# Kernel tuning notes

Measured on AMD Instinct MI355X. Metric: run time of the kernel, lower is better.

## Reference

```python
import jax, jax.numpy as jnp
import numpy as np

INPUT_SIZE = 4
HIDDEN = 2048
OUTPUT_SIZE = 2
NOISE_STD = 0.05
ALPHA = 0.2
RANK = 2
N_SUPPORTS = 2
GDIM = 2 * RANK + INPUT_SIZE  # gaussian_basis_dim default
BATCH = 32
SEQ = 1000


def setup_inputs() -> dict:
    key = jax.random.key(0)
    ks = jax.random.split(key, 8)
    inp = jax.random.normal(ks[0], (BATCH, SEQ, INPUT_SIZE), dtype=jnp.float32)
    noise = jax.random.normal(ks[1], (BATCH, SEQ, HIDDEN), dtype=jnp.float32)
    gaussian_basis = jax.random.normal(ks[2], (GDIM, HIDDEN), dtype=jnp.float32)
    # supports: block indicator masks over hidden units (equal split, weights=None)
    sup = np.zeros((N_SUPPORTS, HIDDEN), dtype=np.float32)
    l = HIDDEN // N_SUPPORTS
    for i in range(N_SUPPORTS):
        sup[i, l * i:l * (i + 1)] = 1.0
    supports = jnp.asarray(sup)
    wi_weights = jax.random.normal(ks[3], (INPUT_SIZE, N_SUPPORTS, GDIM), dtype=jnp.float32)
    m_weights = jax.random.normal(ks[4], (RANK, N_SUPPORTS, GDIM), dtype=jnp.float32) / jnp.sqrt(jnp.float32(HIDDEN))
    n_weights = jax.random.normal(ks[5], (RANK, N_SUPPORTS, GDIM), dtype=jnp.float32) / jnp.sqrt(jnp.float32(HIDDEN))
    wo_weights = jax.random.normal(ks[6], (OUTPUT_SIZE, N_SUPPORTS, GDIM), dtype=jnp.float32) / jnp.float32(HIDDEN)
    wi_biases = jnp.zeros((INPUT_SIZE, N_SUPPORTS), dtype=jnp.float32)
    m_biases = jnp.zeros((RANK, N_SUPPORTS), dtype=jnp.float32)
    n_biases = jnp.zeros((RANK, N_SUPPORTS), dtype=jnp.float32)
    h0_weights = jnp.zeros((N_SUPPORTS, GDIM), dtype=jnp.float32)
    return {
        "input": inp, "noise": noise,
        "wi_weights": wi_weights, "m_weights": m_weights, "n_weights": n_weights,
        "wo_weights": wo_weights, "wi_biases": wi_biases, "m_biases": m_biases,
        "n_biases": n_biases, "h0_weights": h0_weights,
        "gaussian_basis": gaussian_basis, "supports": supports,
    }


def _proxy_params(wi_weights, m_weights, n_weights, wo_weights,
                  wi_biases, m_biases, n_biases, h0_weights,
                  gaussian_basis, supports):
    # (X, S, G) @ (G, H) -> (X, S, H); mask by supports (S, H); sum over S
    def mix(w):
        return jnp.einsum('xsg,gh->xsh', w, gaussian_basis)
    wi = jnp.sum(mix(wi_weights) * supports, axis=1) + wi_biases @ supports      # (I, H)
    m = (jnp.sum(mix(m_weights) * supports, axis=1) + m_biases @ supports).T     # (H, R)
    n = (jnp.sum(mix(n_weights) * supports, axis=1) + n_biases @ supports).T     # (H, R)
    wo = jnp.sum(mix(wo_weights) * supports, axis=1).T                            # (H, O)
    h0 = jnp.sum((h0_weights @ gaussian_basis) * supports, axis=0)                # (H,)
    return wi, m, n, wo, h0


def reference(input, noise, wi_weights, m_weights, n_weights, wo_weights,
              wi_biases, m_biases, n_biases, h0_weights, gaussian_basis, supports):
    wi, m, n, wo, h0 = _proxy_params(wi_weights, m_weights, n_weights, wo_weights,
                                     wi_biases, m_biases, n_biases, h0_weights,
                                     gaussian_basis, supports)
    B = input.shape[0]
    # Precompute external input projection for all steps: (B, T, H)
    xin = jnp.einsum('bti,ih->bth', input, wi)
    h_init = jnp.broadcast_to(h0, (B, h0.shape[0]))
    r_init = jnp.tanh(h_init)

    noise_T = jnp.swapaxes(noise, 0, 1)  # (T, B, H)
    xin_T = jnp.swapaxes(xin, 0, 1)      # (T, B, H)

    def step(carry, xs):
        h, r = carry
        noise_t, xin_t = xs
        h = h + NOISE_STD * noise_t + ALPHA * (-h + (r @ n) @ m.T + xin_t)
        r = jnp.tanh(h)
        return (h, r), r

    _, rs = jax.lax.scan(step, (h_init, r_init), (noise_T, xin_T))  # rs: (T, B, H)
    output = jnp.einsum('tbh,ho->bto', rs, wo)  # (B, T, O)
    return output
```

## Files before the change

kernel.cpp:

```cpp
#include <hip/hip_runtime.h>

#define BATCH 32
#define SEQT 1000
#define INSZ 4
#define HID 2048
#define NOISE_STD 0.05f
#define ALPHA 0.2f
#define ONE_M_ALPHA (1.0f - ALPHA)

#define NTHREADS 512
#define NWAVES 8
#define EPT 4
#define PF 4

typedef float v2f __attribute__((ext_vector_type(2)));

__device__ __forceinline__ v2f vfma(v2f a, v2f b, v2f c) { return a * b + c; }

template<int CTRL>
__device__ __forceinline__ float dpp_add(float x) {
    int s = __builtin_amdgcn_update_dpp(0, __float_as_int(x), CTRL, 0xF, 0xF, true);
    return x + __int_as_float(s);
}

__device__ __forceinline__ float wave_sum64_to_lane63(float x) {
    x = dpp_add<0x111>(x);
    x = dpp_add<0x112>(x);
    x = dpp_add<0x114>(x);
    x = dpp_add<0x118>(x);
    x = dpp_add<0x142>(x);
    x = dpp_add<0x143>(x);
    return x;
}

__device__ __forceinline__ float sum8_to_lane7(float x) {
    x = dpp_add<0x111>(x);
    x = dpp_add<0x112>(x);
    x = dpp_add<0x114>(x);
    return x;
}

__device__ __forceinline__ float read_lane7(float x) {
    return __int_as_float(__builtin_amdgcn_readlane(__float_as_int(x), 7));
}

__device__ __forceinline__ v2f pade_tanh(v2f x) {
    const v2f x2 = x * x;
    const v2f a  = x2 + 105.0f;
    const v2f num = x * vfma(x2, a, v2f{945.0f, 945.0f});
    const v2f c  = vfma(x2, v2f{15.0f, 15.0f}, v2f{420.0f, 420.0f});
    const v2f d  = vfma(x2, c, v2f{945.0f, 945.0f});
    v2f r;
    r.x = num.x * __builtin_amdgcn_rcpf(d.x);
    r.y = num.y * __builtin_amdgcn_rcpf(d.y);
    r.x = fminf(fmaxf(r.x, -1.0f), 1.0f);
    r.y = fminf(fmaxf(r.y, -1.0f), 1.0f);
    return r;
}

__device__ __forceinline__ float pade_tanh_s(float x) {
    const float x2 = x * x;
    const float num = x * fmaf(x2, x2 + 105.0f, 945.0f);
    const float den = fmaf(x2, fmaf(x2, 15.0f, 420.0f), 945.0f);
    float r = num * __builtin_amdgcn_rcpf(den);
    return fminf(fmaxf(r, -1.0f), 1.0f);
}

#define LDS_BARRIER() __asm__ volatile("s_waitcnt lgkmcnt(0)\ns_barrier" ::: "memory")

__global__ __launch_bounds__(NTHREADS)
void rnn_kernel(const float* __restrict__ input,
                const float* __restrict__ noise,
                const float* __restrict__ wi_w,
                const float* __restrict__ m_w,
                const float* __restrict__ n_w,
                const float* __restrict__ wo_w,
                const float* __restrict__ wi_b,
                const float* __restrict__ m_b,
                const float* __restrict__ n_b,
                const float* __restrict__ h0_w,
                const float* __restrict__ gb,
                const float* __restrict__ sup,
                float* __restrict__ out)
{
    __shared__ float4 sIn4[SEQT];
    __shared__ __align__(16) float4 sRed[2][NWAVES];

    const int b    = blockIdx.x;
    const int tid  = threadIdx.x;
    const int wave = tid >> 6;
    const int lane = tid & 63;

    const float4* inRow4 = reinterpret_cast<const float4*>(input + (size_t)b * SEQT * INSZ);
    for (int i = tid; i < SEQT; i += NTHREADS)
        sIn4[i] = inRow4[i];

    v2f wiA[INSZ][2];
    v2f mA0v[2], mA1v[2], n0v[2], n1v[2], wo0v[2], wo1v[2], hv[2];
    v2f q0 = {0.f, 0.f}, q1 = q0, q2 = q0, q3 = q0;

    #pragma unroll
    for (int e = 0; e < EPT; ++e) {
        const int h = tid * 4 + e;
        const int pi = e >> 1, pc = e & 1;
        float gv[8];
        #pragma unroll
        for (int g = 0; g < 8; ++g) gv[g] = gb[g * HID + h];
        const float s0 = sup[h];
        const float s1 = sup[HID + h];

        auto mix = [&](const float* w) -> float {
            float a0 = 0.f, a1 = 0.f;
            #pragma unroll
            for (int g = 0; g < 8; ++g) { a0 += w[g] * gv[g]; a1 += w[8 + g] * gv[g]; }
            return s0 * a0 + s1 * a1;
        };

        #pragma unroll
        for (int i = 0; i < INSZ; ++i)
            wiA[i][pi][pc] = ALPHA * (mix(wi_w + i * 16) + wi_b[i * 2 + 0] * s0 + wi_b[i * 2 + 1] * s1);
        mA0v[pi][pc] = ALPHA * (mix(m_w)      + m_b[0] * s0 + m_b[1] * s1);
        mA1v[pi][pc] = ALPHA * (mix(m_w + 16) + m_b[2] * s0 + m_b[3] * s1);
        const float n0 = mix(n_w)      + n_b[0] * s0 + n_b[1] * s1;
        const float n1 = mix(n_w + 16) + n_b[2] * s0 + n_b[3] * s1;
        const float w0 = mix(wo_w);
        const float w1 = mix(wo_w + 16);
        n0v[pi][pc] = n0;  n1v[pi][pc] = n1;
        wo0v[pi][pc] = w0; wo1v[pi][pc] = w1;
        {
            float a0 = 0.f, a1 = 0.f;
            #pragma unroll
            for (int g = 0; g < 8; ++g) { a0 += h0_w[g] * gv[g]; a1 += h0_w[8 + g] * gv[g]; }
            const float h0v = s0 * a0 + s1 * a1;
            hv[pi][pc] = h0v;
            const float r = pade_tanh_s(h0v);
            q0[pc] += r * n0;  q1[pc] += r * n1;
            q2[pc] += r * w0;  q3[pc] += r * w1;
        }
    }

    const float4* nP4 = reinterpret_cast<const float4*>(noise + (size_t)b * SEQT * HID);
    const int rowStride = HID / 4;
    float4 nb0 = nP4[0 * rowStride + tid];
    float4 nb1 = nP4[1 * rowStride + tid];
    float4 nb2 = nP4[2 * rowStride + tid];
    float4 nb3 = nP4[3 * rowStride + tid];

    float* outRow = out + (size_t)b * SEQT * 2;

    __syncthreads();
    float4 inv0 = sIn4[0];
    float4 inv1 = sIn4[1];
    float4 inv2 = sIn4[2];
    float4 inv3 = sIn4[3];

    float oz = 0.f, ow = 0.f;

    auto do_step = [&](int t, float4& nbuf, float4& invReg) {
        const int par = t & 1;
        const float p0 = q0.x + q0.y, p1 = q1.x + q1.y;
        const float w0 = wave_sum64_to_lane63(p0);
        const float w1 = wave_sum64_to_lane63(p1);
        if (lane == 63) sRed[par][wave] = make_float4(w0, w1, oz, ow);

        LDS_BARRIER();

        const float4 pr = sRed[par][lane & 7];

        const float p2 = q2.x + q2.y, p3 = q3.x + q3.y;
        const float ozn = wave_sum64_to_lane63(p2);
        const float own = wave_sum64_to_lane63(p3);

        const int tpre = (t + PF < SEQT) ? (t + PF) : (SEQT - 1);
        const float4 nv4 = nbuf;
        nbuf = nP4[(size_t)tpre * rowStride + tid];
        const float4 inv = invReg;
        invReg = sIn4[tpre];

        const v2f nlo = {nv4.x, nv4.y}, nhi = {nv4.z, nv4.w};
        v2f acc0 = wiA[0][0] * inv.x;
        v2f acc1 = wiA[0][1] * inv.x;
        acc0 = vfma(wiA[1][0], inv.y, acc0);  acc1 = vfma(wiA[1][1], inv.y, acc1);
        acc0 = vfma(wiA[2][0], inv.z, acc0);  acc1 = vfma(wiA[2][1], inv.z, acc1);
        acc0 = vfma(wiA[3][0], inv.w, acc0);  acc1 = vfma(wiA[3][1], inv.w, acc1);
        acc0 = acc0 + nlo * NOISE_STD;        acc1 = acc1 + nhi * NOISE_STD;
        acc0 = vfma(hv[0], ONE_M_ALPHA, acc0); acc1 = vfma(hv[1], ONE_M_ALPHA, acc1);

        const float y0 = read_lane7(sum8_to_lane7(pr.x));
        const float y1 = read_lane7(sum8_to_lane7(pr.y));

        if (t >= 2 && wave == (t & 7)) {
            const float o0 = sum8_to_lane7(pr.z);
            const float o1 = sum8_to_lane7(pr.w);
            if (lane == 7)
                *reinterpret_cast<float2*>(outRow + (t - 2) * 2) = make_float2(o0, o1);
        }
        oz = ozn; ow = own;

        v2f h2a = vfma(mA1v[0], y1, acc0);
        v2f h2b = vfma(mA1v[1], y1, acc1);
        h2a = vfma(mA0v[0], y0, h2a);
        h2b = vfma(mA0v[1], y0, h2b);
        hv[0] = h2a; hv[1] = h2b;
        const v2f r2a = pade_tanh(h2a);
        const v2f r2b = pade_tanh(h2b);
        q0 = r2a * n0v[0];  q0 = vfma(r2b, n0v[1], q0);
        q1 = r2a * n1v[0];  q1 = vfma(r2b, n1v[1], q1);
        q2 = r2a * wo0v[0]; q2 = vfma(r2b, wo0v[1], q2);
        q3 = r2a * wo1v[0]; q3 = vfma(r2b, wo1v[1], q3);
    };

    for (int t = 0; t < SEQT; t += PF) {
        do_step(t,     nb0, inv0);
        do_step(t + 1, nb1, inv1);
        do_step(t + 2, nb2, inv2);
        do_step(t + 3, nb3, inv3);
    }

    {
        const float p2 = q2.x + q2.y, p3 = q3.x + q3.y;
        const float w2 = wave_sum64_to_lane63(p2);
        const float w3 = wave_sum64_to_lane63(p3);
        if (lane == 63) sRed[0][wave] = make_float4(w2, w3, oz, ow);
        LDS_BARRIER();
        if (wave == 0) {
            const float4 pr = sRed[0][lane & 7];
            const float a999 = sum8_to_lane7(pr.x);
            const float b999 = sum8_to_lane7(pr.y);
            const float a998 = sum8_to_lane7(pr.z);
            const float b998 = sum8_to_lane7(pr.w);
            if (lane == 7) {
                *reinterpret_cast<float2*>(outRow + 998 * 2) = make_float2(a998, b998);
                *reinterpret_cast<float2*>(outRow + 999 * 2) = make_float2(a999, b999);
            }
        }
    }
}

extern "C" void kernel_launch(void* const* d_in, const int* in_sizes, int n_in,
                              void* d_out, int out_size, void* d_ws, size_t ws_size,
                              hipStream_t stream) {
    const float* input = (const float*)d_in[0];
    const float* noise = (const float*)d_in[1];
    const float* wi_w  = (const float*)d_in[2];
    const float* m_w   = (const float*)d_in[3];
    const float* n_w   = (const float*)d_in[4];
    const float* wo_w  = (const float*)d_in[5];
    const float* wi_b  = (const float*)d_in[6];
    const float* m_b   = (const float*)d_in[7];
    const float* n_b   = (const float*)d_in[8];
    const float* h0_w  = (const float*)d_in[9];
    const float* gb    = (const float*)d_in[10];
    const float* sup   = (const float*)d_in[11];
    float* out = (float*)d_out;

    rnn_kernel<<<dim3(BATCH), dim3(NTHREADS), 0, stream>>>(
        input, noise, wi_w, m_w, n_w, wo_w, wi_b, m_b, n_b, h0_w, gb, sup, out);
}
```

Baseline: 871.9 us.

## Hand-code DPP reductions and packed FMA, store full-wave partials to LDS

Replaces the builtin DPP reduction helpers with inline-asm DPP adds that interleave two independent reductions. Every lane now writes its partial to LDS, which removes the lane-63 conditional store, and the cross-wave sum uses a butterfly so every lane holds the result without a readlane. The output partials move to a separate double-buffered LDS array that is read one step later. Inputs are stored pre-duplicated in LDS so that all per-step arithmetic can use explicit v_pk_fma/mul/add. The goal is a shorter serial per-step latency chain; in exchange, inline asm limits compiler scheduling and adds more LDS stores per step.

```diff
diff --git a/kernel.cpp b/kernel.cpp
--- a/kernel.cpp
+++ b/kernel.cpp
@@ -15,44 +15,53 @@
 
 typedef float v2f __attribute__((ext_vector_type(2)));
 
-__device__ __forceinline__ v2f vfma(v2f a, v2f b, v2f c) { return a * b + c; }
-
-template<int CTRL>
-__device__ __forceinline__ float dpp_add(float x) {
-    int s = __builtin_amdgcn_update_dpp(0, __float_as_int(x), CTRL, 0xF, 0xF, true);
-    return x + __int_as_float(s);
-}
-
-__device__ __forceinline__ float wave_sum64_to_lane63(float x) {
-    x = dpp_add<0x111>(x);
-    x = dpp_add<0x112>(x);
-    x = dpp_add<0x114>(x);
-    x = dpp_add<0x118>(x);
-    x = dpp_add<0x142>(x);
-    x = dpp_add<0x143>(x);
-    return x;
-}
-
-__device__ __forceinline__ float sum8_to_lane7(float x) {
-    x = dpp_add<0x111>(x);
-    x = dpp_add<0x112>(x);
-    x = dpp_add<0x114>(x);
-    return x;
-}
-
-__device__ __forceinline__ float read_lane7(float x) {
-    return __int_as_float(__builtin_amdgcn_readlane(__float_as_int(x), 7));
+__device__ __forceinline__ v2f pk_fma(v2f a, v2f b, v2f c) {
+    v2f d; asm("v_pk_fma_f32 %0, %1, %2, %3" : "=v"(d) : "v"(a), "v"(b), "v"(c)); return d;
+}
+__device__ __forceinline__ v2f pk_mul(v2f a, v2f b) {
+    v2f d; asm("v_pk_mul_f32 %0, %1, %2" : "=v"(d) : "v"(a), "v"(b)); return d;
+}
+__device__ __forceinline__ v2f pk_add(v2f a, v2f b) {
+    v2f d; asm("v_pk_add_f32 %0, %1, %2" : "=v"(d) : "v"(a), "v"(b)); return d;
+}
+#define C2(v) (v2f{(v), (v)})
+
+
+__device__ __forceinline__ void tree64_pair(float& a, float& b) {
+    asm("s_nop 1\n\t"
+        "v_add_f32_dpp %0, %0, %0 row_shr:1 row_mask:0xf bank_mask:0xf bound_ctrl:0\n\t"
+        "v_add_f32_dpp %1, %1, %1 row_shr:1 row_mask:0xf bank_mask:0xf bound_ctrl:0\n\t"
+        "v_add_f32_dpp %0, %0, %0 row_shr:2 row_mask:0xf bank_mask:0xf bound_ctrl:0\n\t"
+        "v_add_f32_dpp %1, %1, %1 row_shr:2 row_mask:0xf bank_mask:0xf bound_ctrl:0\n\t"
+        "v_add_f32_dpp %0, %0, %0 row_shr:4 row_mask:0xf bank_mask:0xf bound_ctrl:0\n\t"
+        "v_add_f32_dpp %1, %1, %1 row_shr:4 row_mask:0xf bank_mask:0xf bound_ctrl:0\n\t"
+        "v_add_f32_dpp %0, %0, %0 row_shr:8 row_mask:0xf bank_mask:0xf bound_ctrl:0\n\t"
+        "v_add_f32_dpp %1, %1, %1 row_shr:8 row_mask:0xf bank_mask:0xf bound_ctrl:0\n\t"
+        "v_add_f32_dpp %0, %0, %0 row_bcast:15 row_mask:0xf bank_mask:0xf bound_ctrl:0\n\t"
+        "v_add_f32_dpp %1, %1, %1 row_bcast:15 row_mask:0xf bank_mask:0xf bound_ctrl:0\n\t"
+        "v_add_f32_dpp %0, %0, %0 row_bcast:31 row_mask:0xf bank_mask:0xf bound_ctrl:0\n\t"
+        "v_add_f32_dpp %1, %1, %1 row_bcast:31 row_mask:0xf bank_mask:0xf bound_ctrl:0"
+        : "+v"(a), "+v"(b));
+}
+
+__device__ __forceinline__ void bfly8_pair(float& a, float& b) {
+    asm("s_nop 1\n\t"
+        "v_add_f32_dpp %0, %0, %0 quad_perm:[1,0,3,2] row_mask:0xf bank_mask:0xf\n\t"
+        "v_add_f32_dpp %1, %1, %1 quad_perm:[1,0,3,2] row_mask:0xf bank_mask:0xf\n\t"
+        "v_add_f32_dpp %0, %0, %0 quad_perm:[2,3,0,1] row_mask:0xf bank_mask:0xf\n\t"
+        "v_add_f32_dpp %1, %1, %1 quad_perm:[2,3,0,1] row_mask:0xf bank_mask:0xf\n\t"
+        "v_add_f32_dpp %0, %0, %0 row_half_mirror row_mask:0xf bank_mask:0xf\n\t"
+        "v_add_f32_dpp %1, %1, %1 row_half_mirror row_mask:0xf bank_mask:0xf"
+        : "+v"(a), "+v"(b));
 }
 
 __device__ __forceinline__ v2f pade_tanh(v2f x) {
-    const v2f x2 = x * x;
-    const v2f a  = x2 + 105.0f;
-    const v2f num = x * vfma(x2, a, v2f{945.0f, 945.0f});
-    const v2f c  = vfma(x2, v2f{15.0f, 15.0f}, v2f{420.0f, 420.0f});
-    const v2f d  = vfma(x2, c, v2f{945.0f, 945.0f});
+    const v2f x2  = pk_mul(x, x);
+    const v2f num = pk_mul(x, pk_fma(x2, pk_add(x2, C2(105.0f)), C2(945.0f)));
+    const v2f den = pk_fma(x2, pk_fma(x2, C2(15.0f), C2(420.0f)), C2(945.0f));
     v2f r;
-    r.x = num.x * __builtin_amdgcn_rcpf(d.x);
-    r.y = num.y * __builtin_amdgcn_rcpf(d.y);
+    r.x = num.x * __builtin_amdgcn_rcpf(den.x);
+    r.y = num.y * __builtin_amdgcn_rcpf(den.y);
     r.x = fminf(fmaxf(r.x, -1.0f), 1.0f);
     r.y = fminf(fmaxf(r.y, -1.0f), 1.0f);
     return r;
@@ -83,8 +92,9 @@
                 const float* __restrict__ sup,
                 float* __restrict__ out)
 {
-    __shared__ float4 sIn4[SEQT];
-    __shared__ __align__(16) float4 sRed[2][NWAVES];
+    __shared__ __align__(16) float2 sDup[SEQT][4];
+    __shared__ float2 sW[2][NWAVES][65];
+    __shared__ float2 sO[2][NWAVES][65];
 
     const int b    = blockIdx.x;
     const int tid  = threadIdx.x;
@@ -92,8 +102,13 @@
     const int lane = tid & 63;
 
     const float4* inRow4 = reinterpret_cast<const float4*>(input + (size_t)b * SEQT * INSZ);
-    for (int i = tid; i < SEQT; i += NTHREADS)
-        sIn4[i] = inRow4[i];
+    for (int i = tid; i < SEQT; i += NTHREADS) {
+        const float4 v = inRow4[i];
+        sDup[i][0] = make_float2(v.x, v.x);
+        sDup[i][1] = make_float2(v.y, v.y);
+        sDup[i][2] = make_float2(v.z, v.z);
+        sDup[i][3] = make_float2(v.w, v.w);
+    }
 
     v2f wiA[INSZ][2];
     v2f mA0v[2], mA1v[2], n0v[2], n1v[2], wo0v[2], wo1v[2], hv[2];
@@ -149,90 +164,93 @@
     float* outRow = out + (size_t)b * SEQT * 2;
 
     __syncthreads();
-    float4 inv0 = sIn4[0];
-    float4 inv1 = sIn4[1];
-    float4 inv2 = sIn4[2];
-    float4 inv3 = sIn4[3];
-
-    float oz = 0.f, ow = 0.f;
-
-    auto do_step = [&](int t, float4& nbuf, float4& invReg) {
-        const int par = t & 1;
-        const float p0 = q0.x + q0.y, p1 = q1.x + q1.y;
-        const float w0 = wave_sum64_to_lane63(p0);
-        const float w1 = wave_sum64_to_lane63(p1);
-        if (lane == 63) sRed[par][wave] = make_float4(w0, w1, oz, ow);
+    const float4* dRow = reinterpret_cast<const float4*>(sDup);
+    float4 ivA0 = dRow[0], ivB0 = dRow[1];
+    float4 ivA1 = dRow[2], ivB1 = dRow[3];
+    float4 ivA2 = dRow[4], ivB2 = dRow[5];
+    float4 ivA3 = dRow[6], ivB3 = dRow[7];
+
+    const v2f cNS  = C2(NOISE_STD);
+    const v2f cOMA = C2(ONE_M_ALPHA);
+
+    auto do_step = [&](int t, int PAR, float4& nbuf, float4& ivAreg, float4& ivBreg) {
+        float w0 = q0.x + q0.y;
+        float w1 = q1.x + q1.y;
+        tree64_pair(w0, w1);
+        sW[PAR][wave][lane] = make_float2(w0, w1);
 
         LDS_BARRIER();
 
-        const float4 pr = sRed[par][lane & 7];
-
-        const float p2 = q2.x + q2.y, p3 = q3.x + q3.y;
-        const float ozn = wave_sum64_to_lane63(p2);
-        const float own = wave_sum64_to_lane63(p3);
+        const float2 prw = sW[PAR][lane & 7][63];
+        const float2 pro = sO[PAR ^ 1][lane & 7][63];
+
+        float oz = q2.x + q2.y;
+        float ow = q3.x + q3.y;
+        tree64_pair(oz, ow);
+        sO[PAR][wave][lane] = make_float2(oz, ow);
 
         const int tpre = (t + PF < SEQT) ? (t + PF) : (SEQT - 1);
         const float4 nv4 = nbuf;
         nbuf = nP4[(size_t)tpre * rowStride + tid];
-        const float4 inv = invReg;
-        invReg = sIn4[tpre];
+        const float4 ivA = ivAreg, ivB = ivBreg;
+        ivAreg = dRow[2 * tpre];
+        ivBreg = dRow[2 * tpre + 1];
 
         const v2f nlo = {nv4.x, nv4.y}, nhi = {nv4.z, nv4.w};
-        v2f acc0 = wiA[0][0] * inv.x;
-        v2f acc1 = wiA[0][1] * inv.x;
-        acc0 = vfma(wiA[1][0], inv.y, acc0);  acc1 = vfma(wiA[1][1], inv.y, acc1);
-        acc0 = vfma(wiA[2][0], inv.z, acc0);  acc1 = vfma(wiA[2][1], inv.z, acc1);
-        acc0 = vfma(wiA[3][0], inv.w, acc0);  acc1 = vfma(wiA[3][1], inv.w, acc1);
-        acc0 = acc0 + nlo * NOISE_STD;        acc1 = acc1 + nhi * NOISE_STD;
-        acc0 = vfma(hv[0], ONE_M_ALPHA, acc0); acc1 = vfma(hv[1], ONE_M_ALPHA, acc1);
-
-        const float y0 = read_lane7(sum8_to_lane7(pr.x));
-        const float y1 = read_lane7(sum8_to_lane7(pr.y));
-
-        if (t >= 2 && wave == (t & 7)) {
-            const float o0 = sum8_to_lane7(pr.z);
-            const float o1 = sum8_to_lane7(pr.w);
-            if (lane == 7)
-                *reinterpret_cast<float2*>(outRow + (t - 2) * 2) = make_float2(o0, o1);
-        }
-        oz = ozn; ow = own;
-
-        v2f h2a = vfma(mA1v[0], y1, acc0);
-        v2f h2b = vfma(mA1v[1], y1, acc1);
-        h2a = vfma(mA0v[0], y0, h2a);
-        h2b = vfma(mA0v[1], y0, h2b);
+        const v2f ix = {ivA.x, ivA.y}, iy = {ivA.z, ivA.w};
+        const v2f iz = {ivB.x, ivB.y}, iw = {ivB.z, ivB.w};
+        v2f acc0 = pk_mul(wiA[0][0], ix);
+        v2f acc1 = pk_mul(wiA[0][1], ix);
+        acc0 = pk_fma(wiA[1][0], iy, acc0);  acc1 = pk_fma(wiA[1][1], iy, acc1);
+        acc0 = pk_fma(wiA[2][0], iz, acc0);  acc1 = pk_fma(wiA[2][1], iz, acc1);
+        acc0 = pk_fma(wiA[3][0], iw, acc0);  acc1 = pk_fma(wiA[3][1], iw, acc1);
+        acc0 = pk_fma(nlo, cNS, acc0);       acc1 = pk_fma(nhi, cNS, acc1);
+        acc0 = pk_fma(hv[0], cOMA, acc0);    acc1 = pk_fma(hv[1], cOMA, acc1);
+
+        float y0 = prw.x, y1 = prw.y;
+        bfly8_pair(y0, y1);
+
+        float o0 = pro.x, o1 = pro.y;
+        bfly8_pair(o0, o1);
+        if (t >= 2 && tid == ((t & 7) << 6))
+            *reinterpret_cast<float2*>(outRow + (t - 2) * 2) = make_float2(o0, o1);
+
+        const v2f y0p = {y0, y0}, y1p = {y1, y1};
+        v2f h2a = pk_fma(mA1v[0], y1p, acc0);
+        v2f h2b = pk_fma(mA1v[1], y1p, acc1);
+        h2a = pk_fma(mA0v[0], y0p, h2a);
+        h2b = pk_fma(mA0v[1], y0p, h2b);
         hv[0] = h2a; hv[1] = h2b;
         const v2f r2a = pade_tanh(h2a);
         const v2f r2b = pade_tanh(h2b);
-        q0 = r2a * n0v[0];  q0 = vfma(r2b, n0v[1], q0);
-        q1 = r2a * n1v[0];  q1 = vfma(r2b, n1v[1], q1);
-        q2 = r2a * wo0v[0]; q2 = vfma(r2b, wo0v[1], q2);
-        q3 = r2a * wo1v[0]; q3 = vfma(r2b, wo1v[1], q3);
+        q0 = pk_fma(r2b, n0v[1],  pk_mul(r2a, n0v[0]));
+        q1 = pk_fma(r2b, n1v[1],  pk_mul(r2a, n1v[0]));
+        q2 = pk_fma(r2b, wo0v[1], pk_mul(r2a, wo0v[0]));
+        q3 = pk_fma(r2b, wo1v[1], pk_mul(r2a, wo1v[0]));
     };
 
     for (int t = 0; t < SEQT; t += PF) {
-        do_step(t,     nb0, inv0);
-        do_step(t + 1, nb1, inv1);
-        do_step(t + 2, nb2, inv2);
-        do_step(t + 3, nb3, inv3);
+        do_step(t,     0, nb0, ivA0, ivB0);
+        do_step(t + 1, 1, nb1, ivA1, ivB1);
+        do_step(t + 2, 0, nb2, ivA2, ivB2);
+        do_step(t + 3, 1, nb3, ivA3, ivB3);
     }
 
     {
-        const float p2 = q2.x + q2.y, p3 = q3.x + q3.y;
-        const float w2 = wave_sum64_to_lane63(p2);
-        const float w3 = wave_sum64_to_lane63(p3);
-        if (lane == 63) sRed[0][wave] = make_float4(w2, w3, oz, ow);
+        float a9 = q2.x + q2.y;
+        float b9 = q3.x + q3.y;
+        tree64_pair(a9, b9);
+        sW[0][wave][lane] = make_float2(a9, b9);
         LDS_BARRIER();
-        if (wave == 0) {
-            const float4 pr = sRed[0][lane & 7];
-            const float a999 = sum8_to_lane7(pr.x);
-            const float b999 = sum8_to_lane7(pr.y);
-            const float a998 = sum8_to_lane7(pr.z);
-            const float b998 = sum8_to_lane7(pr.w);
-            if (lane == 7) {
-                *reinterpret_cast<float2*>(outRow + 998 * 2) = make_float2(a998, b998);
-                *reinterpret_cast<float2*>(outRow + 999 * 2) = make_float2(a999, b999);
-            }
+        const float2 pr9 = sW[0][lane & 7][63];
+        const float2 pr8 = sO[1][lane & 7][63];
+        float x9 = pr9.x, y9 = pr9.y;
+        float x8 = pr8.x, y8 = pr8.y;
+        bfly8_pair(x9, y9);
+        bfly8_pair(x8, y8);
+        if (tid == 0) {
+            *reinterpret_cast<float2*>(outRow + 998 * 2) = make_float2(x8, y8);
+            *reinterpret_cast<float2*>(outRow + 999 * 2) = make_float2(x9, y9);
         }
     }
 }
```

Result: faster. 830.4 us (-4.8%).
